# Optimization experiments

Hardware: AMD Instinct MI355X
Metric: run time of the kernel (lower is better)

The kernel has to match this reference:

```python
import jax, jax.numpy as jnp
import numpy as np

B, S, D = 2, 2048, 2048
NH, NKV = 16, 4
HD = D // NH          # 128
Q_DIM = NH * HD       # 2048
KV_DIM = NKV * HD     # 512
N_REP = NH // NKV     # 4


def setup_inputs() -> dict:
    key = jax.random.key(0)
    k1, k2, k3, k4 = jax.random.split(key, 4)
    x = jax.random.normal(k1, (B, S, D), dtype=jnp.float32)
    freqs_cis = jax.random.normal(k2, (S, HD), dtype=jnp.float32)
    Wqkv = jax.random.normal(k3, (Q_DIM + 2 * KV_DIM, D), dtype=jnp.float32) * (D ** -0.5)
    Wo = jax.random.normal(k4, (D, Q_DIM), dtype=jnp.float32) * (Q_DIM ** -0.5)
    return {"x": x, "freqs_cis": freqs_cis, "Wqkv": Wqkv, "Wo": Wo}


def _apply_rope(xq, xk, freqs_cis):
    # xq: [B,S,NH,HD], xk: [B,S,NKV,HD], freqs_cis: [S,HD] viewed as [S,1,HD//2,2]
    f = freqs_cis.reshape(S, 1, HD // 2, 2)
    f0, f1 = f[..., 0], f[..., 1]  # broadcast over batch & heads

    def rot(t):
        shp = t.shape
        tp = t.reshape(*shp[:-1], HD // 2, 2)
        t0, t1 = tp[..., 0], tp[..., 1]
        # row1 = <x, (f0,f1)>;  row0 = <x, (f1,-f0)>  (matches torch flip+negate)
        row1 = t0 * f0 + t1 * f1
        row0 = t0 * f1 - t1 * f0
        return jnp.stack([row0, row1], axis=-1).reshape(shp)

    return rot(xq), rot(xk)


def reference(x, freqs_cis, Wqkv, Wo):
    # Fused QKV projection (exact path: all RLA sketch dims = 0)
    xqkv = jnp.einsum('bsd,od->bso', x, Wqkv)
    xq = xqkv[..., :Q_DIM].reshape(B, S, NH, HD)
    xk = xqkv[..., Q_DIM:Q_DIM + KV_DIM].reshape(B, S, NKV, HD)
    xv = xqkv[..., Q_DIM + KV_DIM:].reshape(B, S, NKV, HD)

    xq, xk = _apply_rope(xq, xk, freqs_cis)

    # [B,H,S,HD]
    xq = xq.transpose(0, 2, 1, 3)
    xk = xk.transpose(0, 2, 1, 3)
    xv = xv.transpose(0, 2, 1, 3)

    # GQA: repeat kv heads n_rep times
    xk = jnp.repeat(xk, N_REP, axis=1)
    xv = jnp.repeat(xv, N_REP, axis=1)

    scale = 1.0 / jnp.sqrt(jnp.asarray(HD, dtype=xq.dtype))
    scores = jnp.einsum('bhqd,bhkd->bhqk', xq, xk) * scale
    causal = jnp.tril(jnp.ones((S, S), dtype=bool))
    scores = jnp.where(causal, scores, jnp.finfo(scores.dtype).min)
    probs = jax.nn.softmax(scores, axis=-1)
    out = jnp.einsum('bhqk,bhkd->bhqd', probs, xv)  # [B,H,S,HD]

    out = out.transpose(0, 2, 1, 3).reshape(B, S, Q_DIM)
    return jnp.einsum('bsq,dq->bsd', out, Wo)
```

## Files before the change

kernel.cpp:

```cpp
#include <hip/hip_runtime.h>
#include <hip/hip_bf16.h>
#include <cstdint>
#include <cstddef>

#define B_ 2
#define S_ 2048
#define NH_ 16
#define NKV_ 4
#define HD_ 128
#define QDIM_ 2048
#define KVDIM_ 512
#define QKV_ 3072

typedef __attribute__((ext_vector_type(8))) short short8;
typedef __attribute__((ext_vector_type(4))) short bhalf4;
typedef __attribute__((ext_vector_type(4))) float float4v;

__device__ __forceinline__ float bf2f(short u) {
  union { unsigned int i; float f; } v;
  v.i = ((unsigned int)(unsigned short)u) << 16;
  return v.f;
}
__device__ __forceinline__ short f2bf(float f) {
  union { float f; unsigned int i; } v; v.f = f;
  unsigned int x = v.i;
  x += 0x7fffu + ((x >> 16) & 1u);
  return (short)(x >> 16);
}

__device__ __forceinline__ void async_copy16(void* lds, const void* g) {
  __builtin_amdgcn_global_load_lds(
      (const __attribute__((address_space(1))) void*)g,
      (__attribute__((address_space(3))) void*)lds, 16, 0, 0);
}

__global__ void f32_to_bf16(const float* __restrict__ src, short* __restrict__ dst,
                            int n8) {
  int id = blockIdx.x * 256 + threadIdx.x;
  if (id >= n8) return;
  const float* f = src + (size_t)id * 8;
  float4v a = *(const float4v*)(f);
  float4v b = *(const float4v*)(f + 4);
  short8 r;
#pragma unroll
  for (int e = 0; e < 4; ++e) { r[e] = f2bf(a[e]); r[4 + e] = f2bf(b[e]); }
  *(short8*)(dst + (size_t)id * 8) = r;
}

template <int N, int K, bool CF32>
__global__ __launch_bounds__(256)
void gemm_nt_bf16(const short* __restrict__ A, const short* __restrict__ Bm,
                  void* __restrict__ Cp) {
  __shared__ __align__(16) short sA[128 * 32];
  __shared__ __align__(16) short sB[128 * 32];
  const int tid = threadIdx.x;
  const int m0 = blockIdx.y * 128, n0 = blockIdx.x * 128;
  const int wave = tid >> 6, lane = tid & 63;
  const int wm = (wave & 1) << 6, wn = (wave >> 1) << 6;
  const int lm = lane & 15, kg = lane >> 4;

  float4v acc[4][4];
#pragma unroll
  for (int i = 0; i < 4; ++i)
#pragma unroll
    for (int j = 0; j < 4; ++j)
      acc[i][j] = (float4v){0.f, 0.f, 0.f, 0.f};

  const int r0 = tid >> 2, c0 = tid & 3;
  const short* gA0 = A + (size_t)(m0 + r0) * K + c0 * 8;
  const short* gA1 = gA0 + (size_t)64 * K;
  const short* gB0 = Bm + (size_t)(n0 + r0) * K + c0 * 8;
  const short* gB1 = gB0 + (size_t)64 * K;
  short* lA0 = sA + tid * 8;
  short* lA1 = sA + 2048 + tid * 8;
  short* lB0 = sB + tid * 8;
  short* lB1 = sB + 2048 + tid * 8;

  for (int k0 = 0; k0 < K; k0 += 32) {
    async_copy16(lA0, gA0 + k0);
    async_copy16(lA1, gA1 + k0);
    async_copy16(lB0, gB0 + k0);
    async_copy16(lB1, gB1 + k0);
    __syncthreads();

    short8 a[4], b[4];
#pragma unroll
    for (int i = 0; i < 4; ++i)
      a[i] = *(const short8*)(sA + (wm + i * 16 + lm) * 32 + kg * 8);
#pragma unroll
    for (int j = 0; j < 4; ++j)
      b[j] = *(const short8*)(sB + (wn + j * 16 + lm) * 32 + kg * 8);
#pragma unroll
    for (int i = 0; i < 4; ++i)
#pragma unroll
      for (int j = 0; j < 4; ++j)
        acc[i][j] = __builtin_amdgcn_mfma_f32_16x16x32_bf16(a[i], b[j], acc[i][j], 0, 0, 0);
    __syncthreads();
  }

#pragma unroll
  for (int i = 0; i < 4; ++i) {
    const int rb = m0 + wm + i * 16 + kg * 4;
#pragma unroll
    for (int j = 0; j < 4; ++j) {
      const int cc = n0 + wn + j * 16 + lm;
#pragma unroll
      for (int r = 0; r < 4; ++r) {
        if constexpr (CF32)
          ((float*)Cp)[(size_t)(rb + r) * N + cc] = acc[i][j][r];
        else
          ((short*)Cp)[(size_t)(rb + r) * N + cc] = f2bf(acc[i][j][r]);
      }
    }
  }
}

__global__ void rope_split(const short* __restrict__ xqkv, const float* __restrict__ freqs,
                           short* __restrict__ Qr, short* __restrict__ Kr,
                           short* __restrict__ Vv) {
  const int id = blockIdx.x * 256 + threadIdx.x;
  const int i = id / (QKV_ / 8);
  const int c8 = id % (QKV_ / 8);
  const int col = c8 * 8;
  const int b = i >> 11, s = i & (S_ - 1);
  short8 xv = *(const short8*)(xqkv + (size_t)i * QKV_ + col);
  if (col < QDIM_ + KVDIM_) {
    int d;
    short* dst;
    float sc;
    if (col < QDIM_) {
      int hh = col >> 7; d = col & 127;
      dst = Qr + ((size_t)(b * NH_ + hh) * S_ + s) * HD_ + d;
      sc = 0.08838834764831845f;
    } else {
      int cc = col - QDIM_;
      int hh = cc >> 7; d = cc & 127;
      dst = Kr + ((size_t)(b * NKV_ + hh) * S_ + s) * HD_ + d;
      sc = 1.0f;
    }
    const float* fp = freqs + (size_t)s * HD_ + d;
    float4v fa = *(const float4v*)(fp);
    float4v fb = *(const float4v*)(fp + 4);
    float ff[8] = {fa[0], fa[1], fa[2], fa[3], fb[0], fb[1], fb[2], fb[3]};
    short8 ov;
#pragma unroll
    for (int pp = 0; pp < 4; ++pp) {
      float t0 = bf2f(xv[2 * pp]), t1 = bf2f(xv[2 * pp + 1]);
      float f0 = ff[2 * pp], f1 = ff[2 * pp + 1];
      ov[2 * pp]     = f2bf((t0 * f1 - t1 * f0) * sc);
      ov[2 * pp + 1] = f2bf((t0 * f0 + t1 * f1) * sc);
    }
    *(short8*)dst = ov;
  } else {
    int cc = col - QDIM_ - KVDIM_;
    int hh = cc >> 7, d = cc & 127;
    *(short8*)(Vv + ((size_t)(b * NKV_ + hh) * S_ + s) * HD_ + d) = xv;
  }
}

__global__ void transpose_v(const short* __restrict__ Vv, short* __restrict__ Vt) {
  __shared__ short t[64][72];
  const int s0 = blockIdx.x * 64, d0 = blockIdx.y * 64;
  const short* src = Vv + (size_t)blockIdx.z * S_ * HD_;
  short* dst = Vt + (size_t)blockIdx.z * S_ * HD_;
  const int tid = threadIdx.x;
#pragma unroll
  for (int c = 0; c < 2; ++c) {
    int ch = tid + 256 * c;
    int row = ch >> 3, kc = ch & 7;
    *(short8*)(&t[row][kc * 8]) =
        *(const short8*)(src + (size_t)(s0 + row) * HD_ + d0 + kc * 8);
  }
  __syncthreads();
#pragma unroll
  for (int c = 0; c < 2; ++c) {
    int ch = tid + 256 * c;
    int drow = ch >> 3, sc = ch & 7;
    short8 w;
#pragma unroll
    for (int j = 0; j < 8; ++j) w[j] = t[sc * 8 + j][drow];
    *(short8*)(dst + (size_t)(d0 + drow) * S_ + s0 + sc * 8) = w;
  }
}

#define TK 64

__global__ __launch_bounds__(256)
void attn_causal(const short* __restrict__ Q, const short* __restrict__ K,
                 const short* __restrict__ Vt, short* __restrict__ O) {
  const int pair = blockIdx.x;
  const int bh = blockIdx.y;
  const int b = bh >> 4, h = bh & 15;
  const int kvh = h >> 2;
  const int tid = threadIdx.x, wave = tid >> 6, lane = tid & 63;
  const int lm = lane & 15, kg = lane >> 4;

  __shared__ __align__(16) short sK[2][TK * HD_];
  __shared__ __align__(16) short sVt[2][HD_ * TK];
  __shared__ __align__(16) short sO[4 * 16 * 128];

  const short* Qb = Q + (size_t)(b * NH_ + h) * S_ * HD_;
  const short* Kb = K + (size_t)(b * NKV_ + kvh) * S_ * HD_;
  const short* Vtb = Vt + (size_t)(b * NKV_ + kvh) * S_ * HD_;

  const int qt0 = pair, qt1 = 31 - pair;
  const int n0 = qt0 + 1;

  auto stage = [&](int k0, int bf) {
#pragma unroll
    for (int c = 0; c < 4; ++c) {
      int ch = tid + 256 * c;
      int row = ch >> 4, kc = ch & 15;
      async_copy16(sK[bf] + ch * 8,
                   Kb + (size_t)(k0 + row) * HD_ + (kc ^ (row & 7)) * 8);
    }
#pragma unroll
    for (int c = 0; c < 4; ++c) {
      int ch = tid + 256 * c;
      int row = ch >> 3, kc = ch & 7;
      async_copy16(sVt[bf] + ch * 8,
                   Vtb + (size_t)row * S_ + k0 + (kc ^ (row & 7)) * 8);
    }
  };

  int qglob = qt0 * 64 + wave * 16 + lm;
  short8 qf[4];
#pragma unroll
  for (int kk = 0; kk < 4; ++kk)
    qf[kk] = *(const short8*)(Qb + (size_t)qglob * HD_ + kk * 32 + kg * 8);
  float mcur = -1e9f, lcur = 0.f;
  float4v o[8];
#pragma unroll
  for (int df = 0; df < 8; ++df) o[df] = (float4v){0.f, 0.f, 0.f, 0.f};

  auto epilogue = [&](int q0w) {
    float inv = 1.f / lcur;
    short* myO = sO + wave * 2048;
#pragma unroll
    for (int df = 0; df < 8; ++df) {
      unsigned int p0 = (unsigned short)f2bf(o[df][0] * inv) |
                        ((unsigned int)(unsigned short)f2bf(o[df][1] * inv) << 16);
      unsigned int p1 = (unsigned short)f2bf(o[df][2] * inv) |
                        ((unsigned int)(unsigned short)f2bf(o[df][3] * inv) << 16);
      int base = lm * 128 + df * 16 + kg * 4;
      *(unsigned int*)(myO + base) = p0;
      *(unsigned int*)(myO + base + 2) = p1;
    }
    int q = lane >> 2, dp = (lane & 3) * 32;
    const size_t rowoff = (size_t)(b * S_ + q0w + q) * QDIM_ + h * HD_ + dp;
#pragma unroll
    for (int e = 0; e < 4; ++e) {
      short8 w = *(const short8*)(myO + q * 128 + dp + e * 8);
      *(short8*)(O + rowoff + e * 8) = w;
    }
  };

  stage(0, 0);

  for (int s = 0; s < 33; ++s) {
    const int bf = s & 1;
    const bool h1 = (s >= n0);
    const int k0 = (h1 ? (s - n0) : s) * TK;
    const bool diag = h1 ? (s == 32) : (s == qt0);

    __syncthreads();
    if (s + 1 < 33) {
      int sn = s + 1;
      int k0n = ((sn >= n0) ? (sn - n0) : sn) * TK;
      stage(k0n, sn & 1);
    }

    float4v sfT[4];
#pragma unroll
    for (int mj = 0; mj < 4; ++mj) sfT[mj] = (float4v){0.f, 0.f, 0.f, 0.f};
#pragma unroll
    for (int kk = 0; kk < 4; ++kk) {
      int kd = kk * 4 + kg;
#pragma unroll
      for (int mj = 0; mj < 4; ++mj) {
        int row = mj * 16 + lm;
        short8 af = *(const short8*)(sK[bf] + row * HD_ + (kd ^ (row & 7)) * 8);
        sfT[mj] = __builtin_amdgcn_mfma_f32_16x16x32_bf16(af, qf[kk], sfT[mj], 0, 0, 0);
      }
    }

    if (diag) {
#pragma unroll
      for (int mj = 0; mj < 4; ++mj)
#pragma unroll
        for (int r = 0; r < 4; ++r) {
          int kcol = k0 + mj * 16 + kg * 4 + r;
          sfT[mj][r] = (kcol <= qglob) ? sfT[mj][r] : -3e38f;
        }
    }

    float mx = -3e38f;
#pragma unroll
    for (int mj = 0; mj < 4; ++mj)
#pragma unroll
      for (int r = 0; r < 4; ++r) mx = fmaxf(mx, sfT[mj][r]);
    mx = fmaxf(mx, __shfl_xor(mx, 16, 64));
    mx = fmaxf(mx, __shfl_xor(mx, 32, 64));
    float mnew = fmaxf(mcur, mx);
    float alpha = __expf(mcur - mnew);
    float rs = 0.f;
    bhalf4 pb[4];
#pragma unroll
    for (int t = 0; t < 4; ++t)
#pragma unroll
      for (int r = 0; r < 4; ++r) {
        float e = __expf(sfT[t][r] - mnew);
        rs += e;
        pb[t][r] = f2bf(e);
      }
    rs += __shfl_xor(rs, 16, 64);
    rs += __shfl_xor(rs, 32, 64);
    mcur = mnew;
    lcur = lcur * alpha + rs;
#pragma unroll
    for (int df = 0; df < 8; ++df)
#pragma unroll
      for (int r = 0; r < 4; ++r) o[df][r] *= alpha;

#pragma unroll
    for (int t = 0; t < 4; ++t) {
      int kc = t * 2 + (kg >> 1);
#pragma unroll
      for (int df = 0; df < 8; ++df) {
        int row = df * 16 + lm;
        bhalf4 va = *(const bhalf4*)(sVt[bf] + row * TK + (kc ^ (row & 7)) * 8 +
                                     (kg & 1) * 4);
        o[df] = __builtin_amdgcn_mfma_f32_16x16x16bf16_1k(va, pb[t], o[df], 0, 0, 0);
      }
    }

    if (s == n0 - 1) {
      epilogue(qt0 * 64 + wave * 16);
      qglob = qt1 * 64 + wave * 16 + lm;
#pragma unroll
      for (int kk = 0; kk < 4; ++kk)
        qf[kk] = *(const short8*)(Qb + (size_t)qglob * HD_ + kk * 32 + kg * 8);
      mcur = -1e9f; lcur = 0.f;
#pragma unroll
      for (int df = 0; df < 8; ++df) o[df] = (float4v){0.f, 0.f, 0.f, 0.f};
    }
  }

  epilogue(qt1 * 64 + wave * 16);
}

extern "C" void kernel_launch(void* const* d_in, const int* in_sizes, int n_in,
                              void* d_out, int out_size, void* d_ws, size_t ws_size,
                              hipStream_t stream) {
  const float* x     = (const float*)d_in[0];
  const float* freqs = (const float*)d_in[1];
  const float* Wqkv  = (const float*)d_in[2];
  const float* Wo    = (const float*)d_in[3];
  float* out = (float*)d_out;

  short* ws     = (short*)d_ws;
  short* xb     = ws;
  short* Wob    = ws;
  short* Wqkvb  = ws + (size_t)4096 * 2048;
  short* xqkv   = Wqkvb + (size_t)QKV_ * 2048;
  short* attn   = xqkv;
  short* Qr     = xqkv + (size_t)4096 * QKV_;
  short* Kr     = Qr + (size_t)B_ * NH_ * S_ * HD_;
  short* Vv     = Kr + (size_t)B_ * NKV_ * S_ * HD_;
  short* Vtg    = Vv + (size_t)B_ * NKV_ * S_ * HD_;

  f32_to_bf16<<<(4096 * 2048 / 8) / 256, 256, 0, stream>>>(x, xb, 4096 * 2048 / 8);
  f32_to_bf16<<<(QKV_ * 2048 / 8) / 256, 256, 0, stream>>>(Wqkv, Wqkvb, QKV_ * 2048 / 8);
  gemm_nt_bf16<QKV_, 2048, false>
      <<<dim3(QKV_ / 128, 4096 / 128), 256, 0, stream>>>(xb, Wqkvb, xqkv);
  f32_to_bf16<<<(2048 * 2048 / 8) / 256, 256, 0, stream>>>(Wo, Wob, 2048 * 2048 / 8);
  rope_split<<<(B_ * S_ * QKV_ / 8) / 256, 256, 0, stream>>>(xqkv, freqs, Qr, Kr, Vv);
  transpose_v<<<dim3(S_ / 64, HD_ / 64, B_ * NKV_), 256, 0, stream>>>(Vv, Vtg);
  attn_causal<<<dim3(16, B_ * NH_), 256, 0, stream>>>(Qr, Kr, Vtg, attn);
  gemm_nt_bf16<2048, 2048, true>
      <<<dim3(2048 / 128, 4096 / 128), 256, 0, stream>>>(attn, Wob, out);
}
```

Measured before the change: 318.5 us.

## Restructure causal attention: one q-tile per block, single-buffer K/V, lazy rescale, exp2

Replaces the paired q-tile scheme with one q-tile per block (1024 blocks, heavy tiles scheduled first), single-buffered K and V in LDS with K/V loads interleaved across two barriers, and occupancy hint of 4 blocks per CU. Folds log2(e) into the Q scale so softmax uses hardware exp2, uses packed bf16 conversion, and skips the output rescale unless the running max grows by more than a threshold. The epilogue writes directly from registers instead of staging through LDS. It trades double-buffered overlap for higher occupancy and removes LDS for the output stage, with less latency hiding per block.

Result: no change. 318.8 us (+0.1%).

```diff
diff --git a/kernel.cpp b/kernel.cpp
--- a/kernel.cpp
+++ b/kernel.cpp
@@ -26,6 +26,18 @@
   unsigned int x = v.i;
   x += 0x7fffu + ((x >> 16) & 1u);
   return (short)(x >> 16);
+}
+
+#if __has_builtin(__builtin_amdgcn_exp2f)
+__device__ __forceinline__ float exp2fast(float x) { return __builtin_amdgcn_exp2f(x); }
+#else
+__device__ __forceinline__ float exp2fast(float x) { return exp2f(x); }
+#endif
+
+__device__ __forceinline__ unsigned int cvt_pk_bf16(float a, float b) {
+  unsigned int r;
+  asm("v_cvt_pk_bf16_f32 %0, %1, %2" : "=v"(r) : "v"(a), "v"(b));
+  return r;
 }
 
 __device__ __forceinline__ void async_copy16(void* lds, const void* g) {
@@ -131,7 +143,7 @@
     if (col < QDIM_) {
       int hh = col >> 7; d = col & 127;
       dst = Qr + ((size_t)(b * NH_ + hh) * S_ + s) * HD_ + d;
-      sc = 0.08838834764831845f;
+      sc = 0.12751744543795287f;
     } else {
       int cc = col - QDIM_;
       int hh = cc >> 7; d = cc & 127;
@@ -185,90 +197,61 @@
 
 #define TK 64
 
-__global__ __launch_bounds__(256)
+__global__ __launch_bounds__(256, 4)
 void attn_causal(const short* __restrict__ Q, const short* __restrict__ K,
                  const short* __restrict__ Vt, short* __restrict__ O) {
-  const int pair = blockIdx.x;
-  const int bh = blockIdx.y;
+  const int bh = blockIdx.x;
+  const int qt = 31 - (int)blockIdx.y;
   const int b = bh >> 4, h = bh & 15;
   const int kvh = h >> 2;
   const int tid = threadIdx.x, wave = tid >> 6, lane = tid & 63;
   const int lm = lane & 15, kg = lane >> 4;
 
-  __shared__ __align__(16) short sK[2][TK * HD_];
-  __shared__ __align__(16) short sVt[2][HD_ * TK];
-  __shared__ __align__(16) short sO[4 * 16 * 128];
+  __shared__ __align__(16) short sK[TK * HD_];
+  __shared__ __align__(16) short sVt[HD_ * TK];
 
   const short* Qb = Q + (size_t)(b * NH_ + h) * S_ * HD_;
   const short* Kb = K + (size_t)(b * NKV_ + kvh) * S_ * HD_;
   const short* Vtb = Vt + (size_t)(b * NKV_ + kvh) * S_ * HD_;
 
-  const int qt0 = pair, qt1 = 31 - pair;
-  const int n0 = qt0 + 1;
-
-  auto stage = [&](int k0, int bf) {
+  auto stageK = [&](int k0) {
 #pragma unroll
     for (int c = 0; c < 4; ++c) {
       int ch = tid + 256 * c;
       int row = ch >> 4, kc = ch & 15;
-      async_copy16(sK[bf] + ch * 8,
+      async_copy16(sK + ch * 8,
                    Kb + (size_t)(k0 + row) * HD_ + (kc ^ (row & 7)) * 8);
     }
+  };
+  auto stageV = [&](int k0) {
 #pragma unroll
     for (int c = 0; c < 4; ++c) {
       int ch = tid + 256 * c;
       int row = ch >> 3, kc = ch & 7;
-      async_copy16(sVt[bf] + ch * 8,
+      async_copy16(sVt + ch * 8,
                    Vtb + (size_t)row * S_ + k0 + (kc ^ (row & 7)) * 8);
     }
   };
 
-  int qglob = qt0 * 64 + wave * 16 + lm;
+  const int qglob = qt * 64 + wave * 16 + lm;
   short8 qf[4];
 #pragma unroll
   for (int kk = 0; kk < 4; ++kk)
     qf[kk] = *(const short8*)(Qb + (size_t)qglob * HD_ + kk * 32 + kg * 8);
+
   float mcur = -1e9f, lcur = 0.f;
   float4v o[8];
 #pragma unroll
   for (int df = 0; df < 8; ++df) o[df] = (float4v){0.f, 0.f, 0.f, 0.f};
 
-  auto epilogue = [&](int q0w) {
-    float inv = 1.f / lcur;
-    short* myO = sO + wave * 2048;
-#pragma unroll
-    for (int df = 0; df < 8; ++df) {
-      unsigned int p0 = (unsigned short)f2bf(o[df][0] * inv) |
-                        ((unsigned int)(unsigned short)f2bf(o[df][1] * inv) << 16);
-      unsigned int p1 = (unsigned short)f2bf(o[df][2] * inv) |
-                        ((unsigned int)(unsigned short)f2bf(o[df][3] * inv) << 16);
-      int base = lm * 128 + df * 16 + kg * 4;
-      *(unsigned int*)(myO + base) = p0;
-      *(unsigned int*)(myO + base + 2) = p1;
-    }
-    int q = lane >> 2, dp = (lane & 3) * 32;
-    const size_t rowoff = (size_t)(b * S_ + q0w + q) * QDIM_ + h * HD_ + dp;
-#pragma unroll
-    for (int e = 0; e < 4; ++e) {
-      short8 w = *(const short8*)(myO + q * 128 + dp + e * 8);
-      *(short8*)(O + rowoff + e * 8) = w;
-    }
-  };
-
-  stage(0, 0);
-
-  for (int s = 0; s < 33; ++s) {
-    const int bf = s & 1;
-    const bool h1 = (s >= n0);
-    const int k0 = (h1 ? (s - n0) : s) * TK;
-    const bool diag = h1 ? (s == 32) : (s == qt0);
+  stageK(0);
+  const int nst = qt + 1;
+  for (int s = 0; s < nst; ++s) {
+    const int k0 = s * TK;
+    const bool diag = (s == qt);
 
     __syncthreads();
-    if (s + 1 < 33) {
-      int sn = s + 1;
-      int k0n = ((sn >= n0) ? (sn - n0) : sn) * TK;
-      stage(k0n, sn & 1);
-    }
+    stageV(k0);
 
     float4v sfT[4];
 #pragma unroll
@@ -279,7 +262,7 @@
 #pragma unroll
       for (int mj = 0; mj < 4; ++mj) {
         int row = mj * 16 + lm;
-        short8 af = *(const short8*)(sK[bf] + row * HD_ + (kd ^ (row & 7)) * 8);
+        short8 af = *(const short8*)(sK + row * HD_ + (kd ^ (row & 7)) * 8);
         sfT[mj] = __builtin_amdgcn_mfma_f32_16x16x32_bf16(af, qf[kk], sfT[mj], 0, 0, 0);
       }
     }
@@ -301,26 +284,38 @@
       for (int r = 0; r < 4; ++r) mx = fmaxf(mx, sfT[mj][r]);
     mx = fmaxf(mx, __shfl_xor(mx, 16, 64));
     mx = fmaxf(mx, __shfl_xor(mx, 32, 64));
-    float mnew = fmaxf(mcur, mx);
-    float alpha = __expf(mcur - mnew);
+    const bool need = (mx > mcur + 4.f);
+    const float mnew = fmaxf(mcur, mx);
+    const float alpha = need ? exp2fast(mcur - mnew) : 1.f;
+    const float m_use = need ? mnew : mcur;
     float rs = 0.f;
     bhalf4 pb[4];
 #pragma unroll
-    for (int t = 0; t < 4; ++t)
-#pragma unroll
-      for (int r = 0; r < 4; ++r) {
-        float e = __expf(sfT[t][r] - mnew);
-        rs += e;
-        pb[t][r] = f2bf(e);
-      }
+    for (int t = 0; t < 4; ++t) {
+      float e0 = exp2fast(sfT[t][0] - m_use);
+      float e1 = exp2fast(sfT[t][1] - m_use);
+      float e2 = exp2fast(sfT[t][2] - m_use);
+      float e3 = exp2fast(sfT[t][3] - m_use);
+      rs += (e0 + e1) + (e2 + e3);
+      union { unsigned int u[2]; bhalf4 v; } pk;
+      pk.u[0] = cvt_pk_bf16(e0, e1);
+      pk.u[1] = cvt_pk_bf16(e2, e3);
+      pb[t] = pk.v;
+    }
     rs += __shfl_xor(rs, 16, 64);
     rs += __shfl_xor(rs, 32, 64);
-    mcur = mnew;
+    mcur = m_use;
     lcur = lcur * alpha + rs;
-#pragma unroll
-    for (int df = 0; df < 8; ++df)
-#pragma unroll
-      for (int r = 0; r < 4; ++r) o[df][r] *= alpha;
+
+    __syncthreads();
+    if (s + 1 < nst) stageK(k0 + TK);
+
+    if (__any(need)) {
+#pragma unroll
+      for (int df = 0; df < 8; ++df)
+#pragma unroll
+        for (int r = 0; r < 4; ++r) o[df][r] *= alpha;
+    }
 
 #pragma unroll
     for (int t = 0; t < 4; ++t) {
@@ -328,25 +323,24 @@
 #pragma unroll
       for (int df = 0; df < 8; ++df) {
         int row = df * 16 + lm;
-        bhalf4 va = *(const bhalf4*)(sVt[bf] + row * TK + (kc ^ (row & 7)) * 8 +
+        bhalf4 va = *(const bhalf4*)(sVt + row * TK + (kc ^ (row & 7)) * 8 +
                                      (kg & 1) * 4);
         o[df] = __builtin_amdgcn_mfma_f32_16x16x16bf16_1k(va, pb[t], o[df], 0, 0, 0);
       }
     }
-
-    if (s == n0 - 1) {
-      epilogue(qt0 * 64 + wave * 16);
-      qglob = qt1 * 64 + wave * 16 + lm;
-#pragma unroll
-      for (int kk = 0; kk < 4; ++kk)
-        qf[kk] = *(const short8*)(Qb + (size_t)qglob * HD_ + kk * 32 + kg * 8);
-      mcur = -1e9f; lcur = 0.f;
-#pragma unroll
-      for (int df = 0; df < 8; ++df) o[df] = (float4v){0.f, 0.f, 0.f, 0.f};
-    }
-  }
-
-  epilogue(qt1 * 64 + wave * 16);
+  }
+
+  const float inv = 1.f / lcur;
+  const size_t rowoff = (size_t)(b * S_ + qglob) * QDIM_ + h * HD_ + kg * 4;
+#pragma unroll
+  for (int df = 0; df < 8; ++df) {
+    bhalf4 w;
+    w[0] = f2bf(o[df][0] * inv);
+    w[1] = f2bf(o[df][1] * inv);
+    w[2] = f2bf(o[df][2] * inv);
+    w[3] = f2bf(o[df][3] * inv);
+    *(bhalf4*)(O + rowoff + df * 16) = w;
+  }
 }
 
 extern "C" void kernel_launch(void* const* d_in, const int* in_sizes, int n_in,
@@ -376,7 +370,7 @@
   f32_to_bf16<<<(2048 * 2048 / 8) / 256, 256, 0, stream>>>(Wo, Wob, 2048 * 2048 / 8);
   rope_split<<<(B_ * S_ * QKV_ / 8) / 256, 256, 0, stream>>>(xqkv, freqs, Qr, Kr, Vv);
   transpose_v<<<dim3(S_ / 64, HD_ / 64, B_ * NKV_), 256, 0, stream>>>(Vv, Vtg);
-  attn_causal<<<dim3(16, B_ * NH_), 256, 0, stream>>>(Qr, Kr, Vtg, attn);
+  attn_causal<<<dim3(32, 32), 256, 0, stream>>>(Qr, Kr, Vtg, attn);
   gemm_nt_bf16<2048, 2048, true>
       <<<dim3(2048 / 128, 4096 / 128), 256, 0, stream>>>(attn, Wob, out);
 }
```
